# Performance work log

Hardware: AMD Instinct MI355X
Metric: run time of the kernel (lower is better)

## Reference

```python
import jax, jax.numpy as jnp
import numpy as np

VOCAB, TAGS, EDIM, HDIM = 128, 8, 256, 1024
B, T = 1024, 128


def setup_inputs() -> dict:
    key = jax.random.key(0)
    ks = jax.random.split(key, 8)
    s = 0.02
    graph_ids = jax.random.randint(ks[0], (B, T), 0, VOCAB)
    emb = jax.random.normal(ks[1], (VOCAB, EDIM), jnp.float32) * s
    emb = emb.at[0].set(0.0)  # padding_idx=0
    W_ih = jax.random.normal(ks[2], (HDIM, EDIM), jnp.float32) * s
    W_hh = jax.random.normal(ks[3], (HDIM, HDIM), jnp.float32) * s
    b_ih = jax.random.normal(ks[4], (HDIM,), jnp.float32) * s
    b_hh = jax.random.normal(ks[5], (HDIM,), jnp.float32) * s
    W_out = jax.random.normal(ks[6], (TAGS, HDIM), jnp.float32) * s
    b_out = jax.random.normal(ks[7], (TAGS,), jnp.float32) * s
    return {"graph_ids": graph_ids, "emb": emb, "W_ih": W_ih, "W_hh": W_hh,
            "b_ih": b_ih, "b_hh": b_hh, "W_out": W_out, "b_out": b_out}


def reference(graph_ids, emb, W_ih, W_hh, b_ih, b_hh, W_out, b_out):
    batch, max_len = graph_ids.shape
    x = emb[graph_ids]                               # [B, T, E]
    mask = (graph_ids != 0).astype(jnp.float32)      # [B, T]
    seq_lengths = mask.sum(axis=1)                   # [B]
    h0 = jnp.zeros((batch, W_hh.shape[0]), x.dtype)

    def step(h, inp):
        x_t, t = inp                                  # x_t: [B, E]
        nh = jnp.tanh(x_t @ W_ih.T + b_ih + h @ W_hh.T + b_hh)
        m = (t < seq_lengths).astype(h.dtype)[:, None]
        h = m * nh + (1.0 - m) * h
        return h, h @ W_out.T + b_out                 # emit tag logits [B, TAGS]

    xs = (jnp.swapaxes(x, 0, 1), jnp.arange(max_len))
    _, ys = jax.lax.scan(step, h0, xs)               # ys: [T, B, TAGS]
    return jnp.swapaxes(ys, 0, 1)                    # [B, T, TAGS]
```

## Files before the change

kernel.cpp:

```cpp
#include <hip/hip_runtime.h>
#include <hip/hip_bf16.h>

typedef __bf16 bf16;
typedef __bf16 bf16x8 __attribute__((ext_vector_type(8)));
typedef float  f32x4  __attribute__((ext_vector_type(4)));

#define TT    128
#define BB    1024
#define VOCAB 128
#define EE    256
#define HH    1024
#define NTAGS 8
#define PW    1034

#define OFF_SW 0
#define OFF_ST (OFF_SW + 64 * PW * 2)
#define OFF_WO (OFF_ST + 64 * 72 * 2)
#define OFF_ID (OFF_WO + NTAGS * 64 * 4)
#define OFF_SL (OFF_ID + 256)
#define LDS_TOTAL (OFF_SL + 256)

#define BARSTRIDE 128

__global__ __launch_bounds__(256) void cvt_k(const float* __restrict__ s,
                                             bf16* __restrict__ d, int n) {
    int i = (blockIdx.x * 256 + threadIdx.x) * 4;
    if (i >= n) return;
    float4 v = *(const float4*)(s + i);
    bf16 o[4] = {(bf16)v.x, (bf16)v.y, (bf16)v.z, (bf16)v.w};
    *(short4*)(d + i) = *(short4*)o;
}

__global__ __launch_bounds__(256) void seqlen_k(const int* __restrict__ ids,
                                                int* __restrict__ sl,
                                                int* __restrict__ idsT) {
    int b = blockIdx.x * 256 + threadIdx.x;
    int c = 0;
    for (int t = 0; t < TT; ++t) {
        int v = ids[b * TT + t];
        idsT[t * BB + b] = v;
        c += (v != 0) ? 1 : 0;
    }
    sl[b] = c;
}

__global__ __launch_bounds__(256) void xp_k(const float* __restrict__ emb,
                                            const float* __restrict__ W_ih,
                                            const float* __restrict__ b_ih,
                                            const float* __restrict__ b_hh,
                                            float* __restrict__ XP) {
    __shared__ float se[EE];
    const int v = blockIdx.x;
    se[threadIdx.x] = emb[v * EE + threadIdx.x];
    __syncthreads();
    const int c0 = threadIdx.x * 4;
    float s0 = 0.f, s1 = 0.f, s2 = 0.f, s3 = 0.f;
    for (int e = 0; e < EE; e += 4) {
        float4 ev = *(const float4*)(se + e);
        float4 w0 = *(const float4*)(W_ih + (c0 + 0) * EE + e);
        float4 w1 = *(const float4*)(W_ih + (c0 + 1) * EE + e);
        float4 w2 = *(const float4*)(W_ih + (c0 + 2) * EE + e);
        float4 w3 = *(const float4*)(W_ih + (c0 + 3) * EE + e);
        s0 += ev.x * w0.x + ev.y * w0.y + ev.z * w0.z + ev.w * w0.w;
        s1 += ev.x * w1.x + ev.y * w1.y + ev.z * w1.z + ev.w * w1.w;
        s2 += ev.x * w2.x + ev.y * w2.y + ev.z * w2.z + ev.w * w2.w;
        s3 += ev.x * w3.x + ev.y * w3.y + ev.z * w3.z + ev.w * w3.w;
    }
    XP[v * HH + c0 + 0] = s0 + b_ih[c0 + 0] + b_hh[c0 + 0];
    XP[v * HH + c0 + 1] = s1 + b_ih[c0 + 1] + b_hh[c0 + 1];
    XP[v * HH + c0 + 2] = s2 + b_ih[c0 + 2] + b_hh[c0 + 2];
    XP[v * HH + c0 + 3] = s3 + b_ih[c0 + 3] + b_hh[c0 + 3];
}

__global__ __launch_bounds__(256, 1)
void rnn_persist(const int*   __restrict__ idsT,
                 const float* __restrict__ XP,
                 const bf16*  __restrict__ Whh,
                 const float* __restrict__ W_out,
                 const int*   __restrict__ sl,
                 bf16* h0, bf16* h1,
                 float* __restrict__ y_part,
                 unsigned* __restrict__ bar)
{
    extern __shared__ __align__(16) char smem[];
    bf16*  sW   = (bf16*)(smem + OFF_SW);
    bf16*  sT   = (bf16*)(smem + OFF_ST);
    float* sWo  = (float*)(smem + OFF_WO);
    int*   sIds = (int*)(smem + OFF_ID);
    int*   sSl  = (int*)(smem + OFF_SL);

    const int tid = threadIdx.x;
    const int xcd = blockIdx.x & 7;
    const int w   = blockIdx.x >> 3;
    const int gm  = xcd * 2 + (w >> 4);
    const int gn  = w & 15;
    const int Mbase = gm * 64, Nbase = gn * 64;

    for (int i = tid; i < 64 * 128; i += 256) {
        int n = i >> 7, g = i & 127;
        *(int4*)(sW + n * PW + g * 8) =
            *(const int4*)(Whh + (size_t)(Nbase + n) * HH + g * 8);
    }
    if (tid < 128) {
        int tg = tid >> 4, c = (tid & 15) * 4;
        *(float4*)(sWo + tg * 64 + c) = *(const float4*)(W_out + tg * HH + Nbase + c);
    }
    if (tid < 64) sSl[tid] = sl[Mbase + tid];
    __syncthreads();

    const int wave = tid >> 6, lane = tid & 63;
    const int quad = lane >> 4, l15 = lane & 15;
    const int wm = (wave >> 1) * 32, wn = (wave & 1) * 32;
    const bf16* pB0 = sW + (wn + l15) * PW;
    const bf16* pB1 = sW + (wn + 16 + l15) * PW;

    unsigned tgt = 0;
    for (int s = 0; s < TT; ++s) {
        const bf16* hp = (s & 1) ? h1 : h0;
        bf16*       hn = (s & 1) ? h0 : h1;

        if (tid < 64) sIds[tid] = idsT[s * BB + Mbase + tid];
        __syncthreads();

        f32x4 acc[2][2];
#pragma unroll
        for (int a = 0; a < 2; ++a)
#pragma unroll
            for (int b = 0; b < 2; ++b) {
                f32x4 z = {0.f, 0.f, 0.f, 0.f};
                acc[a][b] = z;
            }

        const bf16* pa0 = hp + (size_t)(Mbase + wm + l15) * HH + quad * 8;
        const bf16* pa1 = pa0 + (size_t)16 * HH;
        int4 ca0[4], ca1[4];
#pragma unroll
        for (int u = 0; u < 4; ++u) {
            ca0[u] = *(const int4*)(pa0 + u * 32);
            ca1[u] = *(const int4*)(pa1 + u * 32);
        }
#pragma unroll
        for (int jj = 0; jj < 32; jj += 4) {
            int4 na0[4], na1[4];
            if (jj < 28) {
#pragma unroll
                for (int u = 0; u < 4; ++u) {
                    na0[u] = *(const int4*)(pa0 + (jj + 4 + u) * 32);
                    na1[u] = *(const int4*)(pa1 + (jj + 4 + u) * 32);
                }
            }
#pragma unroll
            for (int u = 0; u < 4; ++u) {
                const int j = jj + u;
                bf16x8 b0 = *(const bf16x8*)(pB0 + j * 32 + quad * 8);
                bf16x8 b1 = *(const bf16x8*)(pB1 + j * 32 + quad * 8);
                bf16x8 a0 = __builtin_bit_cast(bf16x8, ca0[u]);
                bf16x8 a1 = __builtin_bit_cast(bf16x8, ca1[u]);
                acc[0][0] = __builtin_amdgcn_mfma_f32_16x16x32_bf16(a0, b0, acc[0][0], 0, 0, 0);
                acc[0][1] = __builtin_amdgcn_mfma_f32_16x16x32_bf16(a0, b1, acc[0][1], 0, 0, 0);
                acc[1][0] = __builtin_amdgcn_mfma_f32_16x16x32_bf16(a1, b0, acc[1][0], 0, 0, 0);
                acc[1][1] = __builtin_amdgcn_mfma_f32_16x16x32_bf16(a1, b1, acc[1][1], 0, 0, 0);
            }
            if (jj < 28) {
#pragma unroll
                for (int u = 0; u < 4; ++u) { ca0[u] = na0[u]; ca1[u] = na1[u]; }
            }
        }

        float xv[2][2][4];
#pragma unroll
        for (int sm = 0; sm < 2; ++sm)
#pragma unroll
            for (int sn = 0; sn < 2; ++sn)
#pragma unroll
                for (int rr = 0; rr < 4; ++rr) {
                    int row = wm + sm * 16 + quad * 4 + rr;
                    int col = wn + sn * 16 + l15;
                    xv[sm][sn][rr] = XP[(size_t)sIds[row] * HH + Nbase + col];
                }
#pragma unroll
        for (int sm = 0; sm < 2; ++sm)
#pragma unroll
            for (int sn = 0; sn < 2; ++sn)
#pragma unroll
                for (int rr = 0; rr < 4; ++rr) {
                    int row = wm + sm * 16 + quad * 4 + rr;
                    int col = wn + sn * 16 + l15;
                    float pre = acc[sm][sn][rr] + xv[sm][sn][rr];
                    pre = fminf(15.f, fmaxf(-15.f, pre));
                    float e = __expf(2.f * pre);
                    float nh = (e - 1.f) / (e + 1.f);
                    bf16 hv;
                    if (s < sSl[row]) hv = (bf16)nh;
                    else hv = hp[(size_t)(Mbase + row) * HH + Nbase + col];
                    sT[row * 72 + col] = hv;
                }
        __syncthreads();

        {
            const int r = tid >> 2, q = tid & 3;
            const bf16* srcp = sT + r * 72 + q * 16;
            int4 w0 = *(const int4*)(srcp);
            int4 w1 = *(const int4*)(srcp + 8);
            unsigned long long u0 = ((unsigned long long)(unsigned)w0.y << 32) | (unsigned)w0.x;
            unsigned long long u1 = ((unsigned long long)(unsigned)w0.w << 32) | (unsigned)w0.z;
            unsigned long long u2 = ((unsigned long long)(unsigned)w1.y << 32) | (unsigned)w1.x;
            unsigned long long u3 = ((unsigned long long)(unsigned)w1.w << 32) | (unsigned)w1.z;
            unsigned long long* hd =
                (unsigned long long*)(hn + (size_t)(Mbase + r) * HH + Nbase + q * 16);
            __hip_atomic_store(hd + 0, u0, __ATOMIC_RELAXED, __HIP_MEMORY_SCOPE_AGENT);
            __hip_atomic_store(hd + 1, u1, __ATOMIC_RELAXED, __HIP_MEMORY_SCOPE_AGENT);
            __hip_atomic_store(hd + 2, u2, __ATOMIC_RELAXED, __HIP_MEMORY_SCOPE_AGENT);
            __hip_atomic_store(hd + 3, u3, __ATOMIC_RELAXED, __HIP_MEMORY_SCOPE_AGENT);

            bf16x8 hv0 = __builtin_bit_cast(bf16x8, w0);
            bf16x8 hv1 = __builtin_bit_cast(bf16x8, w1);
            float lg[NTAGS];
#pragma unroll
            for (int tg = 0; tg < NTAGS; ++tg) {
                const float* ww = sWo + tg * 64 + q * 16;
                float p = 0.f;
#pragma unroll
                for (int j = 0; j < 8; ++j) p += (float)hv0[j] * ww[j];
#pragma unroll
                for (int j = 0; j < 8; ++j) p += (float)hv1[j] * ww[8 + j];
                p += __shfl_xor(p, 1);
                p += __shfl_xor(p, 2);
                lg[tg] = p;
            }
            float* yb = y_part + (((size_t)gn * TT + s) * BB + Mbase + r) * NTAGS
                      + 2 * q;
            yb[0] = lg[2 * q];
            yb[1] = lg[2 * q + 1];
        }

        __syncthreads();
        tgt += 16;
        if (tid == 0) {
            __hip_atomic_fetch_add(&bar[gm * BARSTRIDE], 1u, __ATOMIC_RELAXED,
                                   __HIP_MEMORY_SCOPE_AGENT);
            while (__hip_atomic_load(&bar[gm * BARSTRIDE], __ATOMIC_RELAXED,
                                     __HIP_MEMORY_SCOPE_AGENT) < tgt)
                __builtin_amdgcn_s_sleep(1);
            __builtin_amdgcn_fence(__ATOMIC_ACQUIRE, "agent");
        }
        __syncthreads();
    }
}

__global__ __launch_bounds__(256) void reduce_bias_k(const float* __restrict__ yp,
                                                     const float* __restrict__ b_out,
                                                     float* __restrict__ out) {
    int idx = blockIdx.x * 256 + threadIdx.x;
    int t = idx >> 10, b = idx & 1023;
    float4 s0 = *(const float4*)(b_out);
    float4 s1 = *(const float4*)(b_out + 4);
#pragma unroll
    for (int gn = 0; gn < 16; ++gn) {
        const float* p = yp + (((size_t)gn * TT + t) * BB + b) * NTAGS;
        float4 a = *(const float4*)(p);
        float4 c = *(const float4*)(p + 4);
        s0.x += a.x; s0.y += a.y; s0.z += a.z; s0.w += a.w;
        s1.x += c.x; s1.y += c.y; s1.z += c.z; s1.w += c.w;
    }
    float* o = out + ((size_t)b * TT + t) * NTAGS;
    *(float4*)(o)     = s0;
    *(float4*)(o + 4) = s1;
}

extern "C" void kernel_launch(void* const* d_in, const int* in_sizes, int n_in,
                              void* d_out, int out_size, void* d_ws, size_t ws_size,
                              hipStream_t stream) {
    const int*   ids   = (const int*)d_in[0];
    const float* emb   = (const float*)d_in[1];
    const float* W_ih  = (const float*)d_in[2];
    const float* W_hh  = (const float*)d_in[3];
    const float* b_ih  = (const float*)d_in[4];
    const float* b_hh  = (const float*)d_in[5];
    const float* W_out = (const float*)d_in[6];
    const float* b_out = (const float*)d_in[7];
    float* out = (float*)d_out;

    char* ws = (char*)d_ws;
    size_t off = 0;
    int*      sl     = (int*)(ws + off);      off += 4096;
    int*      idsT   = (int*)(ws + off);      off += (size_t)BB * TT * 4;
    float*    XP     = (float*)(ws + off);    off += (size_t)VOCAB * HH * 4;
    bf16*     Whh16  = (bf16*)(ws + off);     off += (size_t)HH * HH * 2;
    bf16*     h0     = (bf16*)(ws + off);     off += (size_t)BB * HH * 2;
    bf16*     h1     = (bf16*)(ws + off);     off += (size_t)BB * HH * 2;
    float*    y_part = (float*)(ws + off);    off += (size_t)16 * BB * TT * NTAGS * 4;
    unsigned* bar    = (unsigned*)(ws + off); off += 16 * BARSTRIDE * 4;
    if (ws_size < off) return;

    (void)hipMemsetAsync(bar, 0, 16 * BARSTRIDE * 4, stream);
    (void)hipMemsetAsync(h0, 0, (size_t)BB * HH * 2, stream);

    cvt_k<<<(HH * HH / 4 + 255) / 256, 256, 0, stream>>>(W_hh, Whh16, HH * HH);
    xp_k<<<VOCAB, 256, 0, stream>>>(emb, W_ih, b_ih, b_hh, XP);
    seqlen_k<<<4, 256, 0, stream>>>(ids, sl, idsT);

    (void)hipFuncSetAttribute((const void*)rnn_persist,
                              hipFuncAttributeMaxDynamicSharedMemorySize, LDS_TOTAL);
    {
        const int*   a0 = idsT; const float* a1 = XP;  const bf16* a2 = Whh16;
        const float* a3 = W_out; const int*  a4 = sl;
        bf16* a5 = h0; bf16* a6 = h1; float* a7 = y_part; unsigned* a8 = bar;
        void* args[] = {&a0, &a1, &a2, &a3, &a4, &a5, &a6, &a7, &a8};
        (void)hipLaunchCooperativeKernel((const void*)rnn_persist, dim3(256), dim3(256),
                                         args, LDS_TOTAL, stream);
    }

    reduce_bias_k<<<BB * TT / 256, 256, 0, stream>>>(y_part, b_out, out);
}
```

Measured before the change: 1.802 ms.

## Assign row groups by hardware XCC ID and use plain stores with cache invalidate

Each workgroup reads its XCC ID from a hardware register and takes a slot from a per-XCC atomic counter. This guarantees that all 16 blocks sharing an h row-group and barrier counter sit on the same XCD, instead of assuming round-robin dispatch by blockIdx. The per-element agent-scope atomic stores of the new hidden state become plain vector stores. The acquire fence after the barrier becomes a lighter buffer_inv sc0, and a spin cap is added. The aim is to keep barrier and h traffic inside each XCD's L2 and to cut store and fence overhead. The cost is relying on same-XCD L2 coherence for correctness: if the slots on an XCC don't divide cleanly into 32, groups could span XCDs and break.

```diff
diff --git a/kernel.cpp b/kernel.cpp
--- a/kernel.cpp
+++ b/kernel.cpp
@@ -80,7 +80,8 @@
                  const int*   __restrict__ sl,
                  bf16* h0, bf16* h1,
                  float* __restrict__ y_part,
-                 unsigned* __restrict__ bar)
+                 unsigned* __restrict__ bar,
+                 unsigned* __restrict__ xcnt)
 {
     extern __shared__ __align__(16) char smem[];
     bf16*  sW   = (bf16*)(smem + OFF_SW);
@@ -88,18 +89,28 @@
     float* sWo  = (float*)(smem + OFF_WO);
     int*   sIds = (int*)(smem + OFF_ID);
     int*   sSl  = (int*)(smem + OFF_SL);
+    __shared__ int sGrp;
 
     const int tid = threadIdx.x;
-    const int xcd = blockIdx.x & 7;
-    const int w   = blockIdx.x >> 3;
-    const int gm  = xcd * 2 + (w >> 4);
-    const int gn  = w & 15;
+
+    if (tid == 0) {
+        unsigned xcc;
+        asm volatile("s_getreg_b32 %0, hwreg(HW_REG_XCC_ID)" : "=s"(xcc));
+        xcc &= 7;
+        unsigned r = __hip_atomic_fetch_add(&xcnt[xcc], 1u, __ATOMIC_RELAXED,
+                                            __HIP_MEMORY_SCOPE_AGENT);
+        sGrp = (int)(xcc * 32 + (r & 31));
+    }
+    __syncthreads();
+    const int g  = sGrp;
+    const int gm = g >> 4;
+    const int gn = g & 15;
     const int Mbase = gm * 64, Nbase = gn * 64;
 
     for (int i = tid; i < 64 * 128; i += 256) {
-        int n = i >> 7, g = i & 127;
-        *(int4*)(sW + n * PW + g * 8) =
-            *(const int4*)(Whh + (size_t)(Nbase + n) * HH + g * 8);
+        int n = i >> 7, gg = i & 127;
+        *(int4*)(sW + n * PW + gg * 8) =
+            *(const int4*)(Whh + (size_t)(Nbase + n) * HH + gg * 8);
     }
     if (tid < 128) {
         int tg = tid >> 4, c = (tid & 15) * 4;
@@ -202,16 +213,9 @@
             const bf16* srcp = sT + r * 72 + q * 16;
             int4 w0 = *(const int4*)(srcp);
             int4 w1 = *(const int4*)(srcp + 8);
-            unsigned long long u0 = ((unsigned long long)(unsigned)w0.y << 32) | (unsigned)w0.x;
-            unsigned long long u1 = ((unsigned long long)(unsigned)w0.w << 32) | (unsigned)w0.z;
-            unsigned long long u2 = ((unsigned long long)(unsigned)w1.y << 32) | (unsigned)w1.x;
-            unsigned long long u3 = ((unsigned long long)(unsigned)w1.w << 32) | (unsigned)w1.z;
-            unsigned long long* hd =
-                (unsigned long long*)(hn + (size_t)(Mbase + r) * HH + Nbase + q * 16);
-            __hip_atomic_store(hd + 0, u0, __ATOMIC_RELAXED, __HIP_MEMORY_SCOPE_AGENT);
-            __hip_atomic_store(hd + 1, u1, __ATOMIC_RELAXED, __HIP_MEMORY_SCOPE_AGENT);
-            __hip_atomic_store(hd + 2, u2, __ATOMIC_RELAXED, __HIP_MEMORY_SCOPE_AGENT);
-            __hip_atomic_store(hd + 3, u3, __ATOMIC_RELAXED, __HIP_MEMORY_SCOPE_AGENT);
+            bf16* hd = hn + (size_t)(Mbase + r) * HH + Nbase + q * 16;
+            *(int4*)(hd)     = w0;
+            *(int4*)(hd + 8) = w1;
 
             bf16x8 hv0 = __builtin_bit_cast(bf16x8, w0);
             bf16x8 hv1 = __builtin_bit_cast(bf16x8, w1);
@@ -239,10 +243,13 @@
         if (tid == 0) {
             __hip_atomic_fetch_add(&bar[gm * BARSTRIDE], 1u, __ATOMIC_RELAXED,
                                    __HIP_MEMORY_SCOPE_AGENT);
+            unsigned spins = 0;
             while (__hip_atomic_load(&bar[gm * BARSTRIDE], __ATOMIC_RELAXED,
-                                     __HIP_MEMORY_SCOPE_AGENT) < tgt)
+                                     __HIP_MEMORY_SCOPE_AGENT) < tgt) {
                 __builtin_amdgcn_s_sleep(1);
-            __builtin_amdgcn_fence(__ATOMIC_ACQUIRE, "agent");
+                if (++spins > (1u << 24)) break;
+            }
+            asm volatile("buffer_inv sc0" ::: "memory");
         }
         __syncthreads();
     }
@@ -291,9 +298,11 @@
     bf16*     h1     = (bf16*)(ws + off);     off += (size_t)BB * HH * 2;
     float*    y_part = (float*)(ws + off);    off += (size_t)16 * BB * TT * NTAGS * 4;
     unsigned* bar    = (unsigned*)(ws + off); off += 16 * BARSTRIDE * 4;
+    unsigned* xcnt   = (unsigned*)(ws + off); off += 4096;
     if (ws_size < off) return;
 
     (void)hipMemsetAsync(bar, 0, 16 * BARSTRIDE * 4, stream);
+    (void)hipMemsetAsync(xcnt, 0, 4096, stream);
     (void)hipMemsetAsync(h0, 0, (size_t)BB * HH * 2, stream);
 
     cvt_k<<<(HH * HH / 4 + 255) / 256, 256, 0, stream>>>(W_hh, Whh16, HH * HH);
@@ -305,8 +314,9 @@
     {
         const int*   a0 = idsT; const float* a1 = XP;  const bf16* a2 = Whh16;
         const float* a3 = W_out; const int*  a4 = sl;
-        bf16* a5 = h0; bf16* a6 = h1; float* a7 = y_part; unsigned* a8 = bar;
-        void* args[] = {&a0, &a1, &a2, &a3, &a4, &a5, &a6, &a7, &a8};
+        bf16* a5 = h0; bf16* a6 = h1; float* a7 = y_part;
+        unsigned* a8 = bar; unsigned* a9 = xcnt;
+        void* args[] = {&a0, &a1, &a2, &a3, &a4, &a5, &a6, &a7, &a8, &a9};
         (void)hipLaunchCooperativeKernel((const void*)rnn_persist, dim3(256), dim3(256),
                                          args, LDS_TOTAL, stream);
     }
```

Measured after the change: 1.610 ms. 1.12x faster.
